# Performance work log

Measured on AMD Instinct MI355X. Metric: run time of the kernel, lower is better.

The kernel has to match this reference:

```python
import jax, jax.numpy as jnp
import numpy as np

B, S, HID = 2, 1024, 2048
H, HK, D = 32, 4, 128
G = H // HK
EPS = 1e-6
SCALE = 1.0 / np.sqrt(D)
ROPE_THETA = 1000000.0


def _rope_tables(seq_len, dim, theta):
    inv_freq = 1.0 / (theta ** (np.arange(0, dim, 2, dtype=np.float32) / dim))
    t = np.arange(seq_len, dtype=np.float32)
    freqs = np.outer(t, inv_freq)                      # [S, D/2]
    emb = np.concatenate([freqs, freqs], axis=-1)       # [S, D]
    return (jnp.asarray(np.cos(emb))[None, :, None, :],
            jnp.asarray(np.sin(emb))[None, :, None, :])  # [1,S,1,D]


def setup_inputs() -> dict:
    key = jax.random.key(0)
    k1, k2, k3 = jax.random.split(key, 3)
    cos, sin = _rope_tables(S, D, ROPE_THETA)
    return {
        "hidden_states": jax.random.normal(k1, (B, S, HID), jnp.float32),
        "cos": cos,
        "sin": sin,
        "w_qkv": jax.random.normal(k2, (HID, (H + 2 * HK) * D), jnp.float32) * 0.02,
        "q_norm_w": jnp.ones((D,), jnp.float32),
        "k_norm_w": jnp.ones((D,), jnp.float32),
        "w_o": jax.random.normal(k3, (H * D, HID), jnp.float32) * 0.02,
    }


def _rms_norm(x, w):
    xf = x.astype(jnp.float32)
    var = jnp.mean(xf * xf, axis=-1, keepdims=True)
    return (w * (xf * jax.lax.rsqrt(var + EPS))).astype(x.dtype)


def _rotate_half(x):
    x1, x2 = jnp.split(x, 2, axis=-1)
    return jnp.concatenate([-x2, x1], axis=-1)


def reference(hidden_states, cos, sin, w_qkv, q_norm_w, k_norm_w, w_o):
    b, s, _ = hidden_states.shape
    qkv = hidden_states @ w_qkv                          # [B,S,(H+2HK)*D]
    q, k, v = jnp.split(qkv, [H * D, (H + HK) * D], axis=-1)
    q = q.reshape(b, s, H, D)
    k = k.reshape(b, s, HK, D)
    v = v.reshape(b, s, HK, D)
    # per-head RMSNorm on q/k, then rotary (BSH layout)
    q = _rms_norm(q, q_norm_w)
    k = _rms_norm(k, k_norm_w)
    q = q * cos + _rotate_half(q) * sin
    k = k * cos + _rotate_half(k) * sin
    # grouped-query causal SDPA (prefill path, sparse_mode=2)
    qg = q.reshape(b, s, HK, G, D)
    scores = jnp.einsum("bqkgd,bskd->bkgqs", qg, k) * SCALE  # [B,HK,G,S,S]
    causal = jnp.tril(jnp.ones((s, s), bool))
    scores = jnp.where(causal, scores, jnp.finfo(scores.dtype).min)
    probs = jax.nn.softmax(scores, axis=-1)
    ctx = jnp.einsum("bkgqs,bskd->bqkgd", probs, v)          # [B,S,HK,G,D]
    ctx = ctx.reshape(b, s, H * D)
    return ctx @ w_o                                          # [B,S,HID]
```

## Files before the change

### kernel.cpp

```cpp
#include <hip/hip_runtime.h>

#define B_   2
#define S_   1024
#define HID_ 2048
#define H_   32
#define HK_  4
#define D_   128
#define NQKV ((H_ + 2 * HK_) * D_)
#define TOK  (B_ * S_)

typedef short bf16x8  __attribute__((ext_vector_type(8)));
typedef short short4v __attribute__((ext_vector_type(4)));
typedef float f32x4   __attribute__((ext_vector_type(4)));
typedef int   i32x4   __attribute__((ext_vector_type(4)));

__device__ inline short f2bf(float f) {
  unsigned u = __builtin_bit_cast(unsigned, f);
  u += 0x7fffu + ((u >> 16) & 1u);
  return (short)(u >> 16);
}

__device__ __forceinline__ void gld_lds16(const short* g, short* l) {
  __builtin_amdgcn_global_load_lds((__attribute__((address_space(1))) void*)g,
                                   (__attribute__((address_space(3))) void*)l, 16, 0, 0);
}

__global__ __launch_bounds__(256) void cast_f32_bf16(const float* __restrict__ in,
                                                     short* __restrict__ out, int n4) {
  int i = blockIdx.x * 256 + threadIdx.x;
  if (i >= n4) return;
  f32x4 v = ((const f32x4*)in)[i];
  short4v o;
  o[0] = f2bf(v[0]); o[1] = f2bf(v[1]); o[2] = f2bf(v[2]); o[3] = f2bf(v[3]);
  ((short4v*)out)[i] = o;
}

__global__ __launch_bounds__(256) void transpose_cast(const float* __restrict__ in,
                                                      short* __restrict__ out,
                                                      int K, int N) {
  __shared__ float tile[32][33];
  int nb = blockIdx.x * 32, kb = blockIdx.y * 32;
  int c = threadIdx.x & 31, r0 = threadIdx.x >> 5;
#pragma unroll
  for (int i = 0; i < 4; i++) {
    int r = r0 + i * 8;
    tile[r][c] = in[(size_t)(kb + r) * N + nb + c];
  }
  __syncthreads();
#pragma unroll
  for (int i = 0; i < 4; i++) {
    int r = r0 + i * 8;
    out[(size_t)(nb + r) * K + kb + c] = f2bf(tile[c][r]);
  }
}

__global__ __launch_bounds__(256) void gemm_bt128(const short* __restrict__ A,
                                                  const short* __restrict__ Bt,
                                                  float* __restrict__ C,
                                                  int M, int N, int Kfull, int klen) {
  const int tid  = threadIdx.x;
  const int m0   = blockIdx.y * 128;
  const int n0   = blockIdx.x * 128;
  const int kz0  = blockIdx.z * klen;
  const int w    = tid >> 6, lane = tid & 63;
  const int quad = lane >> 4, l16 = lane & 15;
  const int wm   = (w >> 1) * 64, wn = (w & 1) * 64;

  __shared__ short As[128 * 64];
  __shared__ short Bs[128 * 64];

  const f32x4 z = {0.f, 0.f, 0.f, 0.f};
  f32x4 acc[4][4];
#pragma unroll
  for (int i = 0; i < 4; i++)
#pragma unroll
    for (int j = 0; j < 4; j++) acc[i][j] = z;

  const int srow = lane >> 3;
  const int lc   = (lane & 7) ^ srow;

  for (int kk = 0; kk < klen; kk += 64) {
    const int k0 = kz0 + kk;
#pragma unroll
    for (int i = 0; i < 4; i++) {
      int rb = w * 32 + i * 8;
      gld_lds16(&A [(size_t)(m0 + rb + srow) * Kfull + k0 + lc * 8], &As[rb * 64]);
      gld_lds16(&Bt[(size_t)(n0 + rb + srow) * Kfull + k0 + lc * 8], &Bs[rb * 64]);
    }
    __syncthreads();
#pragma unroll
    for (int kb = 0; kb < 2; kb++) {
      const int pc = ((kb * 4 + quad) ^ (l16 & 7)) * 8;
      bf16x8 a[4], b[4];
#pragma unroll
      for (int f = 0; f < 4; f++) {
        a[f] = *(const bf16x8*)&As[(wm + f * 16 + l16) * 64 + pc];
        b[f] = *(const bf16x8*)&Bs[(wn + f * 16 + l16) * 64 + pc];
      }
#pragma unroll
      for (int fi = 0; fi < 4; fi++)
#pragma unroll
        for (int fj = 0; fj < 4; fj++)
          acc[fi][fj] = __builtin_amdgcn_mfma_f32_16x16x32_bf16(a[fi], b[fj], acc[fi][fj], 0, 0, 0);
    }
    __syncthreads();
  }

  float* Cz = C + (size_t)blockIdx.z * M * N;
#pragma unroll
  for (int fi = 0; fi < 4; fi++) {
    int row0 = m0 + wm + fi * 16 + quad * 4;
#pragma unroll
    for (int fj = 0; fj < 4; fj++) {
      int col = n0 + wn + fj * 16 + l16;
#pragma unroll
      for (int r = 0; r < 4; r++)
        Cz[(size_t)(row0 + r) * N + col] = acc[fi][fj][r];
    }
  }
}

__global__ __launch_bounds__(256) void add2(const float* __restrict__ a,
                                            const float* __restrict__ b,
                                            float* __restrict__ c, int n4) {
  int i = blockIdx.x * 256 + threadIdx.x;
  if (i >= n4) return;
  f32x4 va = ((const f32x4*)a)[i], vb = ((const f32x4*)b)[i];
  ((f32x4*)c)[i] = va + vb;
}

__global__ __launch_bounds__(64) void rmsnorm_rope_qk(const float* __restrict__ qkv,
                                                      const float* __restrict__ cosT,
                                                      const float* __restrict__ sinT,
                                                      const float* __restrict__ qw,
                                                      const float* __restrict__ kw,
                                                      short* __restrict__ Qb,
                                                      short* __restrict__ Kb) {
  int t    = blockIdx.x;
  int hd   = blockIdx.y;
  int b    = t >> 10;
  int s    = t & (S_ - 1);
  int lane = threadIdx.x;
  const float QSC = 0.08838834764831845f * 1.4426950408889634f;
  const float* base;
  const float* w;
  short* dst;
  float osc;
  if (hd < H_) {
    base = qkv + (size_t)t * NQKV + hd * D_;
    w = qw; osc = QSC;
    dst = Qb + (((size_t)b * H_ + hd) * S_ + s) * D_;
  } else {
    base = qkv + (size_t)t * NQKV + H_ * D_ + (hd - H_) * D_;
    w = kw; osc = 1.0f;
    dst = Kb + (((size_t)b * HK_ + (hd - H_)) * S_ + s) * D_;
  }
  float x1 = base[lane], x2 = base[lane + 64];
  float ss = x1 * x1 + x2 * x2;
#pragma unroll
  for (int off = 32; off > 0; off >>= 1) ss += __shfl_xor(ss, off, 64);
  float rn = rsqrtf(ss * (1.0f / 128.0f) + 1e-6f);
  float y1 = x1 * rn * w[lane], y2 = x2 * rn * w[lane + 64];
  float c1 = cosT[s * D_ + lane],      s1 = sinT[s * D_ + lane];
  float c2 = cosT[s * D_ + lane + 64], s2 = sinT[s * D_ + lane + 64];
  dst[lane]      = f2bf((y1 * c1 - y2 * s1) * osc);
  dst[lane + 64] = f2bf((y2 * c2 + y1 * s2) * osc);
}

__global__ __launch_bounds__(256) void v_pack(const float* __restrict__ qkv,
                                              short* __restrict__ Vt) {
  int bk = blockIdx.x;
  int s0 = blockIdx.y * 64;
  int d  = threadIdx.x & 127;
  int sg = threadIdx.x >> 7;
  int b = bk >> 2, kh = bk & 3;
  short buf[32];
  const float* src = qkv + ((size_t)(b * S_ + s0 + sg * 32)) * NQKV + (H_ + HK_) * D_ + kh * D_ + d;
#pragma unroll
  for (int sj = 0; sj < 32; sj++)
    buf[sj] = f2bf(src[(size_t)sj * NQKV]);
  short* dst = Vt + ((size_t)bk * D_ + d) * S_ + s0 + sg * 32;
#pragma unroll
  for (int i = 0; i < 4; i++) ((i32x4*)dst)[i] = ((const i32x4*)buf)[i];
}

__global__ __launch_bounds__(256) void attn_mfma2(const short* __restrict__ Qb,
                                                  const short* __restrict__ Kb,
                                                  const short* __restrict__ Vt,
                                                  short* __restrict__ ctx) {
  const int qt = (int)gridDim.x - 1 - blockIdx.x;
  const int h  = blockIdx.y;
  const int b  = blockIdx.z;
  const int kh = h >> 3;
  const int q0 = qt * 128;
  const int tid = threadIdx.x, w = tid >> 6, lane = tid & 63;
  const int quad = lane >> 4, l16 = lane & 15;

  __shared__ short Ks[128 * 64];
  __shared__ short Vs[144 * 64];
  __shared__ short Ps[4][2][16 * 72];

  for (int i = tid; i < 16 * 64; i += 256) Vs[128 * 64 + i] = (short)0x3F80;

  const short* Qbase = Qb + (((size_t)b * H_ + h) * S_ + q0) * D_;
  bf16x8 aq[2][4];
#pragma unroll
  for (int fi = 0; fi < 2; fi++)
#pragma unroll
    for (int kb = 0; kb < 4; kb++)
      aq[fi][kb] = *(const bf16x8*)&Qbase[(size_t)(fi * 64 + w * 16 + l16) * D_ + kb * 32 + quad * 8];

  const f32x4 z = {0.f, 0.f, 0.f, 0.f};
  f32x4 O[2][9];
#pragma unroll
  for (int fi = 0; fi < 2; fi++)
#pragma unroll
    for (int n = 0; n < 9; n++) O[fi][n] = z;
  float m_r[2][4] = {{-1e30f, -1e30f, -1e30f, -1e30f}, {-1e30f, -1e30f, -1e30f, -1e30f}};

  const short* Kbase = Kb + ((size_t)(b * HK_ + kh) * S_) * D_;
  const short* Vbase = Vt + ((size_t)(b * HK_ + kh) * D_) * S_;

  const int srow = lane >> 3;
  const int lc   = (lane & 7) ^ srow;

  const int nkt = 2 * qt + 2;
  for (int kt = 0; kt < nkt; kt++) {
    const int k0 = kt * 64;
    __syncthreads();
#pragma unroll
    for (int i = 0; i < 4; i++) {
      int rb = w * 32 + i * 8;
      int rr = rb + srow;
      gld_lds16(&Kbase[(size_t)(k0 + (rr >> 1)) * D_ + (rr & 1) * 64 + lc * 8], &Ks[rb * 64]);
      gld_lds16(&Vbase[(size_t)rr * S_ + k0 + lc * 8], &Vs[rb * 64]);
    }
    __syncthreads();

#pragma unroll
    for (int fi = 0; fi < 2; fi++) {
      if (kt > 2 * qt + fi) continue;

      f32x4 Sc[4] = {z, z, z, z};
#pragma unroll
      for (int kb = 0; kb < 4; kb++) {
        const int h2 = kb >> 1;
        const int c7 = (kb & 1) * 4 + quad;
#pragma unroll
        for (int nb = 0; nb < 4; nb++) {
          int rr = 2 * (nb * 16 + l16) + h2;
          bf16x8 bk = *(const bf16x8*)&Ks[rr * 64 + (c7 ^ (rr & 7)) * 8];
          Sc[nb] = __builtin_amdgcn_mfma_f32_16x16x32_bf16(aq[fi][kb], bk, Sc[nb], 0, 0, 0);
        }
      }
      if (kt == 2 * qt + fi) {
#pragma unroll
        for (int nb = 0; nb < 4; nb++) {
          int col = k0 + nb * 16 + l16;
#pragma unroll
          for (int r = 0; r < 4; r++) {
            int row = q0 + fi * 64 + w * 16 + quad * 4 + r;
            if (col > row) Sc[nb][r] = -1e30f;
          }
        }
      }

      float alpha[4];
#pragma unroll
      for (int r = 0; r < 4; r++) {
        float mx = fmaxf(fmaxf(Sc[0][r], Sc[1][r]), fmaxf(Sc[2][r], Sc[3][r]));
#pragma unroll
        for (int off = 1; off < 16; off <<= 1) mx = fmaxf(mx, __shfl_xor(mx, off, 64));
        float mn = fmaxf(m_r[fi][r], mx);
        alpha[r] = exp2f(m_r[fi][r] - mn);
        m_r[fi][r] = mn;
#pragma unroll
        for (int nb = 0; nb < 4; nb++) Sc[nb][r] = exp2f(Sc[nb][r] - mn);
      }

#pragma unroll
      for (int nb = 0; nb < 4; nb++)
#pragma unroll
        for (int r = 0; r < 4; r++)
          Ps[w][fi][(quad * 4 + r) * 72 + nb * 16 + l16] = f2bf(Sc[nb][r]);

#pragma unroll
      for (int n = 0; n < 9; n++)
#pragma unroll
        for (int r = 0; r < 4; r++) O[fi][n][r] *= alpha[r];

#pragma unroll
      for (int kb2 = 0; kb2 < 2; kb2++) {
        bf16x8 ap = *(const bf16x8*)&Ps[w][fi][l16 * 72 + kb2 * 32 + quad * 8];
        const int c7 = kb2 * 4 + quad;
#pragma unroll
        for (int nb2 = 0; nb2 < 9; nb2++) {
          int d = nb2 * 16 + l16;
          bf16x8 bv = *(const bf16x8*)&Vs[d * 64 + (c7 ^ (d & 7)) * 8];
          O[fi][nb2] = __builtin_amdgcn_mfma_f32_16x16x32_bf16(ap, bv, O[fi][nb2], 0, 0, 0);
        }
      }
    }
  }

#pragma unroll
  for (int fi = 0; fi < 2; fi++)
#pragma unroll
    for (int r = 0; r < 4; r++) {
      float inv = 1.0f / O[fi][8][r];
      size_t row = (size_t)(b * S_ + q0 + fi * 64 + w * 16 + quad * 4 + r);
      short* dst = ctx + row * (H_ * D_) + h * D_;
#pragma unroll
      for (int nb2 = 0; nb2 < 8; nb2++)
        dst[nb2 * 16 + l16] = f2bf(O[fi][nb2][r] * inv);
    }
}

extern "C" void kernel_launch(void* const* d_in, const int* in_sizes, int n_in,
                              void* d_out, int out_size, void* d_ws, size_t ws_size,
                              hipStream_t stream) {
  (void)in_sizes; (void)n_in; (void)out_size; (void)ws_size;
  const float* hidden = (const float*)d_in[0];
  const float* cosT   = (const float*)d_in[1];
  const float* sinT   = (const float*)d_in[2];
  const float* wqkv   = (const float*)d_in[3];
  const float* qnw    = (const float*)d_in[4];
  const float* knw    = (const float*)d_in[5];
  const float* wo     = (const float*)d_in[6];
  float* out = (float*)d_out;

  char* ws = (char*)d_ws;
  float* qkv = (float*)(ws);
  short* hb  = (short*)(ws + 41943040);
  short* wT  = (short*)(ws + 41943040 + 8388608);
  short* ctx = (short*)(ws + 41943040 + 8388608 + 20971520);
  short* Kb  = hb;
  short* Vt  = hb + 1048576;
  short* Qb  = wT;
  float* part = (float*)ws;

  cast_f32_bf16<<<4096, 256, 0, stream>>>(hidden, hb, TOK * HID_ / 4);
  transpose_cast<<<dim3(NQKV / 32, HID_ / 32), 256, 0, stream>>>(wqkv, wT, HID_, NQKV);
  gemm_bt128<<<dim3(NQKV / 128, TOK / 128, 1), 256, 0, stream>>>(hb, wT, qkv, TOK, NQKV, HID_, HID_);
  rmsnorm_rope_qk<<<dim3(TOK, H_ + HK_), 64, 0, stream>>>(qkv, cosT, sinT, qnw, knw, Qb, Kb);
  v_pack<<<dim3(B_ * HK_, S_ / 64), 256, 0, stream>>>(qkv, Vt);
  attn_mfma2<<<dim3(S_ / 128, H_, B_), 256, 0, stream>>>(Qb, Kb, Vt, ctx);
  transpose_cast<<<dim3(HID_ / 32, (H_ * D_) / 32), 256, 0, stream>>>(wo, wT, H_ * D_, HID_);
  gemm_bt128<<<dim3(HID_ / 128, TOK / 128, 2), 256, 0, stream>>>(ctx, wT, part, TOK, HID_, H_ * D_, (H_ * D_) / 2);
  add2<<<(TOK * HID_ / 4 + 255) / 256, 256, 0, stream>>>(part, part + (size_t)TOK * HID_, out, TOK * HID_ / 4);
}
```

Measured before the change: 366.1 us.

## Share K/V LDS fragments across both query sub-tiles and interleave tile order

The attention kernel now loads each K and V fragment from LDS once and feeds it to the MFMAs of both 64-row query sub-tiles, instead of running two separate passes. This halves the LDS reads for K and V. The K tile layout in LDS changes to a row-contiguous half split with a simpler swizzle. The kernel also sets launch bounds to 3 waves per SIMD and interleaves long and short causal q-tiles to balance the load. In exchange, register pressure rises because two score accumulators are live at once, and when only the second sub-tile is active the shared score MFMAs for the first sub-tile are computed and then discarded.

```diff
diff --git a/kernel.cpp b/kernel.cpp
--- a/kernel.cpp
+++ b/kernel.cpp
@@ -184,11 +184,12 @@
   for (int i = 0; i < 4; i++) ((i32x4*)dst)[i] = ((const i32x4*)buf)[i];
 }
 
-__global__ __launch_bounds__(256) void attn_mfma2(const short* __restrict__ Qb,
-                                                  const short* __restrict__ Kb,
-                                                  const short* __restrict__ Vt,
-                                                  short* __restrict__ ctx) {
-  const int qt = (int)gridDim.x - 1 - blockIdx.x;
+__global__ __launch_bounds__(256, 3) void attn_mfma3(const short* __restrict__ Qb,
+                                                     const short* __restrict__ Kb,
+                                                     const short* __restrict__ Vt,
+                                                     short* __restrict__ ctx) {
+  const int qmap[8] = {7, 0, 6, 1, 5, 2, 4, 3};
+  const int qt = qmap[blockIdx.x & 7];
   const int h  = blockIdx.y;
   const int b  = blockIdx.z;
   const int kh = h >> 3;
@@ -232,27 +233,35 @@
     for (int i = 0; i < 4; i++) {
       int rb = w * 32 + i * 8;
       int rr = rb + srow;
-      gld_lds16(&Kbase[(size_t)(k0 + (rr >> 1)) * D_ + (rr & 1) * 64 + lc * 8], &Ks[rb * 64]);
+      gld_lds16(&Kbase[(size_t)(k0 + (rr & 63)) * D_ + (rr >> 6) * 64 + lc * 8], &Ks[rb * 64]);
       gld_lds16(&Vbase[(size_t)rr * S_ + k0 + lc * 8], &Vs[rb * 64]);
     }
     __syncthreads();
 
+    const bool do0 = (kt <= 2 * qt);
+
+    f32x4 Sc[2][4];
+#pragma unroll
+    for (int fi = 0; fi < 2; fi++)
+#pragma unroll
+      for (int nb = 0; nb < 4; nb++) Sc[fi][nb] = z;
+#pragma unroll
+    for (int kb = 0; kb < 4; kb++) {
+      const int c  = kb * 4 + quad;
+      const int c7 = c & 7;
+      const int rbase = (c >> 3) * 64;
+#pragma unroll
+      for (int nb = 0; nb < 4; nb++) {
+        int rr = rbase + nb * 16 + l16;
+        bf16x8 bk = *(const bf16x8*)&Ks[rr * 64 + (c7 ^ (l16 & 7)) * 8];
+        Sc[0][nb] = __builtin_amdgcn_mfma_f32_16x16x32_bf16(aq[0][kb], bk, Sc[0][nb], 0, 0, 0);
+        Sc[1][nb] = __builtin_amdgcn_mfma_f32_16x16x32_bf16(aq[1][kb], bk, Sc[1][nb], 0, 0, 0);
+      }
+    }
+
 #pragma unroll
     for (int fi = 0; fi < 2; fi++) {
-      if (kt > 2 * qt + fi) continue;
-
-      f32x4 Sc[4] = {z, z, z, z};
-#pragma unroll
-      for (int kb = 0; kb < 4; kb++) {
-        const int h2 = kb >> 1;
-        const int c7 = (kb & 1) * 4 + quad;
-#pragma unroll
-        for (int nb = 0; nb < 4; nb++) {
-          int rr = 2 * (nb * 16 + l16) + h2;
-          bf16x8 bk = *(const bf16x8*)&Ks[rr * 64 + (c7 ^ (rr & 7)) * 8];
-          Sc[nb] = __builtin_amdgcn_mfma_f32_16x16x32_bf16(aq[fi][kb], bk, Sc[nb], 0, 0, 0);
-        }
-      }
+      if (fi == 0 && !do0) continue;
       if (kt == 2 * qt + fi) {
 #pragma unroll
         for (int nb = 0; nb < 4; nb++) {
@@ -260,45 +269,44 @@
 #pragma unroll
           for (int r = 0; r < 4; r++) {
             int row = q0 + fi * 64 + w * 16 + quad * 4 + r;
-            if (col > row) Sc[nb][r] = -1e30f;
+            if (col > row) Sc[fi][nb][r] = -1e30f;
           }
         }
       }
-
       float alpha[4];
 #pragma unroll
       for (int r = 0; r < 4; r++) {
-        float mx = fmaxf(fmaxf(Sc[0][r], Sc[1][r]), fmaxf(Sc[2][r], Sc[3][r]));
+        float mx = fmaxf(fmaxf(Sc[fi][0][r], Sc[fi][1][r]), fmaxf(Sc[fi][2][r], Sc[fi][3][r]));
 #pragma unroll
         for (int off = 1; off < 16; off <<= 1) mx = fmaxf(mx, __shfl_xor(mx, off, 64));
         float mn = fmaxf(m_r[fi][r], mx);
         alpha[r] = exp2f(m_r[fi][r] - mn);
         m_r[fi][r] = mn;
 #pragma unroll
-        for (int nb = 0; nb < 4; nb++) Sc[nb][r] = exp2f(Sc[nb][r] - mn);
-      }
-
+        for (int nb = 0; nb < 4; nb++) Sc[fi][nb][r] = exp2f(Sc[fi][nb][r] - mn);
+      }
 #pragma unroll
       for (int nb = 0; nb < 4; nb++)
 #pragma unroll
         for (int r = 0; r < 4; r++)
-          Ps[w][fi][(quad * 4 + r) * 72 + nb * 16 + l16] = f2bf(Sc[nb][r]);
-
+          Ps[w][fi][(quad * 4 + r) * 72 + nb * 16 + l16] = f2bf(Sc[fi][nb][r]);
 #pragma unroll
       for (int n = 0; n < 9; n++)
 #pragma unroll
         for (int r = 0; r < 4; r++) O[fi][n][r] *= alpha[r];
-
-#pragma unroll
-      for (int kb2 = 0; kb2 < 2; kb2++) {
-        bf16x8 ap = *(const bf16x8*)&Ps[w][fi][l16 * 72 + kb2 * 32 + quad * 8];
-        const int c7 = kb2 * 4 + quad;
-#pragma unroll
-        for (int nb2 = 0; nb2 < 9; nb2++) {
-          int d = nb2 * 16 + l16;
-          bf16x8 bv = *(const bf16x8*)&Vs[d * 64 + (c7 ^ (d & 7)) * 8];
-          O[fi][nb2] = __builtin_amdgcn_mfma_f32_16x16x32_bf16(ap, bv, O[fi][nb2], 0, 0, 0);
-        }
+    }
+
+#pragma unroll
+    for (int kb2 = 0; kb2 < 2; kb2++) {
+      bf16x8 ap0 = *(const bf16x8*)&Ps[w][0][l16 * 72 + kb2 * 32 + quad * 8];
+      bf16x8 ap1 = *(const bf16x8*)&Ps[w][1][l16 * 72 + kb2 * 32 + quad * 8];
+      const int c7 = kb2 * 4 + quad;
+#pragma unroll
+      for (int nb2 = 0; nb2 < 9; nb2++) {
+        int d = nb2 * 16 + l16;
+        bf16x8 bv = *(const bf16x8*)&Vs[d * 64 + (c7 ^ (d & 7)) * 8];
+        if (do0) O[0][nb2] = __builtin_amdgcn_mfma_f32_16x16x32_bf16(ap0, bv, O[0][nb2], 0, 0, 0);
+        O[1][nb2] = __builtin_amdgcn_mfma_f32_16x16x32_bf16(ap1, bv, O[1][nb2], 0, 0, 0);
       }
     }
   }
@@ -344,7 +352,7 @@
   gemm_bt128<<<dim3(NQKV / 128, TOK / 128, 1), 256, 0, stream>>>(hb, wT, qkv, TOK, NQKV, HID_, HID_);
   rmsnorm_rope_qk<<<dim3(TOK, H_ + HK_), 64, 0, stream>>>(qkv, cosT, sinT, qnw, knw, Qb, Kb);
   v_pack<<<dim3(B_ * HK_, S_ / 64), 256, 0, stream>>>(qkv, Vt);
-  attn_mfma2<<<dim3(S_ / 128, H_, B_), 256, 0, stream>>>(Qb, Kb, Vt, ctx);
+  attn_mfma3<<<dim3(S_ / 128, H_, B_), 256, 0, stream>>>(Qb, Kb, Vt, ctx);
   transpose_cast<<<dim3(HID_ / 32, (H_ * D_) / 32), 256, 0, stream>>>(wo, wT, H_ * D_, HID_);
   gemm_bt128<<<dim3(HID_ / 128, TOK / 128, 2), 256, 0, stream>>>(ctx, wT, part, TOK, HID_, H_ * D_, (H_ * D_) / 2);
   add2<<<(TOK * HID_ / 4 + 255) / 256, 256, 0, stream>>>(part, part + (size_t)TOK * HID_, out, TOK * HID_ / 4);
```

Measured after the change: 411.7 us. +12.4%, slower.
